# Kernel optimization log

Measured on AMD Instinct MI355X. Metric: run time of the kernel, lower is better.

The kernel has to match this reference:

```python
import jax, jax.numpy as jnp
import numpy as np
import math

D_MODEL = 1024
NUM_HEADS = 16
HEAD_DIM = D_MODEL // NUM_HEADS
N = 16384


def setup_inputs() -> dict:
    key = jax.random.key(0)
    ks = jax.random.split(key, 11)
    s = 1.0 / math.sqrt(D_MODEL)
    return {
        "q": jax.random.normal(ks[0], (N, D_MODEL), jnp.float32),
        "k": jax.random.normal(ks[1], (N, D_MODEL), jnp.float32),
        "v": jax.random.normal(ks[2], (N, D_MODEL), jnp.float32),
        "Wq": jax.random.normal(ks[3], (D_MODEL, D_MODEL), jnp.float32) * s,
        "bq": jnp.zeros((D_MODEL,), jnp.float32),
        "Wk": jax.random.normal(ks[4], (D_MODEL, D_MODEL), jnp.float32) * s,
        "bk": jnp.zeros((D_MODEL,), jnp.float32),
        "Wv": jax.random.normal(ks[5], (D_MODEL, D_MODEL), jnp.float32) * s,
        "bv": jnp.zeros((D_MODEL,), jnp.float32),
        "Wo": jax.random.normal(ks[6], (D_MODEL, D_MODEL), jnp.float32) * s,
        "bo": jnp.zeros((D_MODEL,), jnp.float32),
    }


def reference(q, k, v, Wq, bq, Wk, bk, Wv, bv, Wo, bo):
    scale = math.sqrt(HEAD_DIM)
    # Linear projections (torch Linear: x @ W.T + b), then view [N, H, Dh]
    qh = (q @ Wq.T + bq).reshape(-1, NUM_HEADS, HEAD_DIM)
    kh = (k @ Wk.T + bk).reshape(-1, NUM_HEADS, HEAD_DIM)
    vh = (v @ Wv.T + bv).reshape(-1, NUM_HEADS, HEAD_DIM)
    # NOTE: faithful to source — attention is over the HEADS axis per token:
    # scores [N, H, H]
    scores = jnp.einsum("nhd,ngd->nhg", qh, kh) / scale
    attn = jax.nn.softmax(scores, axis=-1)
    out = jnp.einsum("nhg,ngd->nhd", attn, vh).reshape(-1, D_MODEL)
    return out @ Wo.T + bo
```

## Files before the change

kernel.cpp:

```cpp
#include <hip/hip_runtime.h>

#define NTOK 16384
#define DM 1024
#define BM 128
#define BN 128
#define BK 64

typedef _Float16 h16;
typedef __attribute__((ext_vector_type(8))) _Float16 half8;
typedef __attribute__((ext_vector_type(4))) _Float16 half4;
typedef __attribute__((ext_vector_type(4))) float floatx4;

__device__ __forceinline__ unsigned lds_off(unsigned r, unsigned c) {
  return r * 128u + ((((c >> 3) ^ r) & 7u) << 4) + (c & 7u) * 2u;
}

__device__ __forceinline__ uint2 f4h4(float4 f) {
  unsigned short a = __builtin_bit_cast(unsigned short, (h16)f.x);
  unsigned short b = __builtin_bit_cast(unsigned short, (h16)f.y);
  unsigned short c = __builtin_bit_cast(unsigned short, (h16)f.z);
  unsigned short d = __builtin_bit_cast(unsigned short, (h16)f.w);
  uint2 r;
  r.x = (unsigned)a | ((unsigned)b << 16);
  r.y = (unsigned)c | ((unsigned)d << 16);
  return r;
}

template <bool AHALF, bool OHALF>
__global__ __launch_bounds__(256, 4) void gemm_h(const void* __restrict__ Aptr,
                                                 const float* __restrict__ W,
                                                 const float* __restrict__ bias,
                                                 void* __restrict__ Cptr) {
  __shared__ __align__(16) char smem[32768];
  char* Ap = smem;
  char* Bp = smem + 16384;

  const int tid = threadIdx.x;

  const int bid = (int)(blockIdx.x + gridDim.x * blockIdx.y);
  const int xcd = bid & 7, ch = bid >> 3;
  const int m0 = (xcd * 16 + (ch >> 3)) * BM;
  const int n0 = (ch & 7) * BN;

  const int lane = tid & 63;
  const int wave = tid >> 6;
  const int wm = (wave >> 1) * 64;
  const int wn = (wave & 1) * 64;
  const int fr = lane & 15;
  const int fq = lane >> 4;

  floatx4 acc[4][4] = {};

  const int rb = tid >> 4, c4 = tid & 15;
  const int rA = tid >> 3, c8 = tid & 7;

  const float* wg = W + (long)(n0 + rb) * DM + c4 * 4;
  const float* agf = AHALF ? nullptr : (const float*)Aptr + (long)(m0 + rb) * DM + c4 * 4;
  const h16* agh = AHALF ? (const h16*)Aptr + (long)(m0 + rA) * DM + c8 * 8 : nullptr;

  for (int kt = 0; kt < DM; kt += BK) {
    if constexpr (AHALF) {
#pragma unroll
      for (int i = 0; i < 4; ++i) {
        uint4 u = *(const uint4*)(agh + (long)i * 32 * DM + kt);
        *(uint4*)(Ap + lds_off(rA + i * 32, c8 * 8)) = u;
      }
    } else {
#pragma unroll
      for (int i = 0; i < 8; ++i) {
        float4 fa = *(const float4*)(agf + (long)i * 16 * DM + kt);
        *(uint2*)(Ap + lds_off(rb + i * 16, c4 * 4)) = f4h4(fa);
      }
    }
#pragma unroll
    for (int i = 0; i < 8; ++i) {
      float4 fb = *(const float4*)(wg + (long)i * 16 * DM + kt);
      *(uint2*)(Bp + lds_off(rb + i * 16, c4 * 4)) = f4h4(fb);
    }
    __syncthreads();

#pragma unroll
    for (int ks = 0; ks < 2; ++ks) {
      half8 af[4], bf[4];
#pragma unroll
      for (int i = 0; i < 4; ++i) {
        af[i] = *(half8*)(Ap + lds_off(wm + i * 16 + fr, ks * 32 + fq * 8));
        bf[i] = *(half8*)(Bp + lds_off(wn + i * 16 + fr, ks * 32 + fq * 8));
      }
#pragma unroll
      for (int mi = 0; mi < 4; ++mi)
#pragma unroll
        for (int ni = 0; ni < 4; ++ni)
          acc[mi][ni] = __builtin_amdgcn_mfma_f32_16x16x32_f16(af[mi], bf[ni], acc[mi][ni], 0, 0, 0);
    }
    __syncthreads();
  }

#pragma unroll
  for (int ni = 0; ni < 4; ++ni) {
    const int col = n0 + wn + ni * 16 + fr;
    const float bv = bias[col];
#pragma unroll
    for (int mi = 0; mi < 4; ++mi) {
      const int row0 = m0 + wm + mi * 16 + fq * 4;
#pragma unroll
      for (int j = 0; j < 4; ++j) {
        const float val = acc[mi][ni][j] + bv;
        if constexpr (OHALF)
          ((h16*)Cptr)[(long)(row0 + j) * DM + col] = (h16)val;
        else
          ((float*)Cptr)[(long)(row0 + j) * DM + col] = val;
      }
    }
  }
}

__global__ __launch_bounds__(256) void attn_heads_h(h16* __restrict__ Q,
                                                    const h16* __restrict__ K,
                                                    const h16* __restrict__ V) {
  __shared__ float qs[16][68];
  __shared__ float ks[16][68];
  __shared__ float vs[16][68];
  __shared__ float pw[16][17];
  const int t = blockIdx.x;
  const int tid = threadIdx.x;
  const long base = (long)t * DM + tid * 4;
  const int h = tid >> 4;
  const int d0 = (tid & 15) * 4;

  {
    half4 fq = *(const half4*)(Q + base);
    half4 fk = *(const half4*)(K + base);
    half4 fv = *(const half4*)(V + base);
    *(float4*)&qs[h][d0] = make_float4((float)fq[0], (float)fq[1], (float)fq[2], (float)fq[3]);
    *(float4*)&ks[h][d0] = make_float4((float)fk[0], (float)fk[1], (float)fk[2], (float)fk[3]);
    *(float4*)&vs[h][d0] = make_float4((float)fv[0], (float)fv[1], (float)fv[2], (float)fv[3]);
  }
  __syncthreads();

  const int g = tid & 15;
  float s = 0.f;
#pragma unroll
  for (int d = 0; d < 64; ++d) s += qs[h][d] * ks[g][d];
  s *= 0.125f;

  float mx = s;
#pragma unroll
  for (int off = 8; off > 0; off >>= 1) mx = fmaxf(mx, __shfl_xor(mx, off, 16));
  float e = __expf(s - mx);
  float den = e;
#pragma unroll
  for (int off = 8; off > 0; off >>= 1) den += __shfl_xor(den, off, 16);
  pw[h][g] = e / den;
  __syncthreads();

  float4 o = make_float4(0.f, 0.f, 0.f, 0.f);
#pragma unroll
  for (int g2 = 0; g2 < 16; ++g2) {
    const float p = pw[h][g2];
    o.x += p * vs[g2][d0 + 0];
    o.y += p * vs[g2][d0 + 1];
    o.z += p * vs[g2][d0 + 2];
    o.w += p * vs[g2][d0 + 3];
  }
  half4 oh;
  oh[0] = (h16)o.x; oh[1] = (h16)o.y; oh[2] = (h16)o.z; oh[3] = (h16)o.w;
  *(half4*)(Q + base) = oh;
}

extern "C" void kernel_launch(void* const* d_in, const int* in_sizes, int n_in,
                              void* d_out, int out_size, void* d_ws, size_t ws_size,
                              hipStream_t stream) {
  const float* q  = (const float*)d_in[0];
  const float* k  = (const float*)d_in[1];
  const float* v  = (const float*)d_in[2];
  const float* Wq = (const float*)d_in[3];
  const float* bq = (const float*)d_in[4];
  const float* Wk = (const float*)d_in[5];
  const float* bk = (const float*)d_in[6];
  const float* Wv = (const float*)d_in[7];
  const float* bv = (const float*)d_in[8];
  const float* Wo = (const float*)d_in[9];
  const float* bo = (const float*)d_in[10];

  h16* Qp = (h16*)d_ws;
  h16* Kp = Qp + (size_t)NTOK * DM;
  h16* Vp = Kp + (size_t)NTOK * DM;

  dim3 ggrid(DM / BN, NTOK / BM);
  dim3 gblk(256);

  gemm_h<false, true><<<ggrid, gblk, 0, stream>>>(q, Wq, bq, Qp);
  gemm_h<false, true><<<ggrid, gblk, 0, stream>>>(k, Wk, bk, Kp);
  gemm_h<false, true><<<ggrid, gblk, 0, stream>>>(v, Wv, bv, Vp);
  attn_heads_h<<<dim3(NTOK), gblk, 0, stream>>>(Qp, Kp, Vp);
  gemm_h<true, false><<<ggrid, gblk, 0, stream>>>(Qp, Wo, bo, (float*)d_out);
}
```

Baseline: 526.4 us.

## Pre-convert inputs and weights to fp16, load GEMM tiles via direct global-to-LDS

Adds separate conversion kernels that cast q/k/v and all four weight matrices to fp16 up front. The GEMM is rewritten to take fp16 operands only and to fill LDS with global_load_lds 16-byte direct copies using an XOR-swizzled lane mapping, instead of register-staged float loads converted in-loop. This is meant to cut per-tile conversion work and VGPR staging inside the GEMM, and to halve the bytes each GEMM reads. The cost is an extra full read/write pass over the activations and more workspace, with projection outputs reusing the converted input buffers.

```diff
diff --git a/kernel.cpp b/kernel.cpp
--- a/kernel.cpp
+++ b/kernel.cpp
@@ -15,22 +15,16 @@
   return r * 128u + ((((c >> 3) ^ r) & 7u) << 4) + (c & 7u) * 2u;
 }
 
-__device__ __forceinline__ uint2 f4h4(float4 f) {
-  unsigned short a = __builtin_bit_cast(unsigned short, (h16)f.x);
-  unsigned short b = __builtin_bit_cast(unsigned short, (h16)f.y);
-  unsigned short c = __builtin_bit_cast(unsigned short, (h16)f.z);
-  unsigned short d = __builtin_bit_cast(unsigned short, (h16)f.w);
-  uint2 r;
-  r.x = (unsigned)a | ((unsigned)b << 16);
-  r.y = (unsigned)c | ((unsigned)d << 16);
-  return r;
-}
-
-template <bool AHALF, bool OHALF>
-__global__ __launch_bounds__(256, 4) void gemm_h(const void* __restrict__ Aptr,
-                                                 const float* __restrict__ W,
-                                                 const float* __restrict__ bias,
-                                                 void* __restrict__ Cptr) {
+__device__ __forceinline__ void gload16(const h16* g, char* l) {
+  __builtin_amdgcn_global_load_lds((const __attribute__((address_space(1))) unsigned*)g,
+                                   (__attribute__((address_space(3))) unsigned*)l, 16, 0, 0);
+}
+
+template <bool OHALF>
+__global__ __launch_bounds__(256, 4) void gemm_hh(const h16* __restrict__ A,
+                                                  const h16* __restrict__ W,
+                                                  const float* __restrict__ bias,
+                                                  void* __restrict__ Cptr) {
   __shared__ __align__(16) char smem[32768];
   char* Ap = smem;
   char* Bp = smem + 16384;
@@ -51,31 +45,18 @@
 
   floatx4 acc[4][4] = {};
 
-  const int rb = tid >> 4, c4 = tid & 15;
-  const int rA = tid >> 3, c8 = tid & 7;
-
-  const float* wg = W + (long)(n0 + rb) * DM + c4 * 4;
-  const float* agf = AHALF ? nullptr : (const float*)Aptr + (long)(m0 + rb) * DM + c4 * 4;
-  const h16* agh = AHALF ? (const h16*)Aptr + (long)(m0 + rA) * DM + c8 * 8 : nullptr;
+  const int lr = lane >> 3;
+  const int lc = (lane & 7) ^ lr;
+  const h16* ag = A + (long)(m0 + wave * 32 + lr) * DM + lc * 8;
+  const h16* wg = W + (long)(n0 + wave * 32 + lr) * DM + lc * 8;
+  char* const alds = Ap + wave * 4096;
+  char* const blds = Bp + wave * 4096;
 
   for (int kt = 0; kt < DM; kt += BK) {
-    if constexpr (AHALF) {
-#pragma unroll
-      for (int i = 0; i < 4; ++i) {
-        uint4 u = *(const uint4*)(agh + (long)i * 32 * DM + kt);
-        *(uint4*)(Ap + lds_off(rA + i * 32, c8 * 8)) = u;
-      }
-    } else {
-#pragma unroll
-      for (int i = 0; i < 8; ++i) {
-        float4 fa = *(const float4*)(agf + (long)i * 16 * DM + kt);
-        *(uint2*)(Ap + lds_off(rb + i * 16, c4 * 4)) = f4h4(fa);
-      }
-    }
-#pragma unroll
-    for (int i = 0; i < 8; ++i) {
-      float4 fb = *(const float4*)(wg + (long)i * 16 * DM + kt);
-      *(uint2*)(Bp + lds_off(rb + i * 16, c4 * 4)) = f4h4(fb);
+#pragma unroll
+    for (int i = 0; i < 4; ++i) {
+      gload16(ag + (long)(i * 8) * DM + kt, alds + i * 1024);
+      gload16(wg + (long)(i * 8) * DM + kt, blds + i * 1024);
     }
     __syncthreads();
 
@@ -113,6 +94,35 @@
       }
     }
   }
+}
+
+__global__ __launch_bounds__(256) void cvt3(const float* __restrict__ a, const float* __restrict__ b,
+                                            const float* __restrict__ c, h16* __restrict__ oa,
+                                            h16* __restrict__ ob, h16* __restrict__ oc) {
+  const long i = ((long)blockIdx.x * 256 + threadIdx.x) * 8;
+  const float* s = blockIdx.y == 0 ? a : blockIdx.y == 1 ? b : c;
+  h16* d = blockIdx.y == 0 ? oa : blockIdx.y == 1 ? ob : oc;
+  float4 f0 = *(const float4*)(s + i);
+  float4 f1 = *(const float4*)(s + i + 4);
+  half8 h;
+  h[0] = (h16)f0.x; h[1] = (h16)f0.y; h[2] = (h16)f0.z; h[3] = (h16)f0.w;
+  h[4] = (h16)f1.x; h[5] = (h16)f1.y; h[6] = (h16)f1.z; h[7] = (h16)f1.w;
+  *(half8*)(d + i) = h;
+}
+
+__global__ __launch_bounds__(256) void cvtW(const float* __restrict__ a, const float* __restrict__ b,
+                                            const float* __restrict__ c, const float* __restrict__ e,
+                                            h16* __restrict__ oa, h16* __restrict__ ob,
+                                            h16* __restrict__ oc, h16* __restrict__ oe) {
+  const long i = ((long)blockIdx.x * 256 + threadIdx.x) * 8;
+  const float* s = blockIdx.y == 0 ? a : blockIdx.y == 1 ? b : blockIdx.y == 2 ? c : e;
+  h16* d = blockIdx.y == 0 ? oa : blockIdx.y == 1 ? ob : blockIdx.y == 2 ? oc : oe;
+  float4 f0 = *(const float4*)(s + i);
+  float4 f1 = *(const float4*)(s + i + 4);
+  half8 h;
+  h[0] = (h16)f0.x; h[1] = (h16)f0.y; h[2] = (h16)f0.z; h[3] = (h16)f0.w;
+  h[4] = (h16)f1.x; h[5] = (h16)f1.y; h[6] = (h16)f1.z; h[7] = (h16)f1.w;
+  *(half8*)(d + i) = h;
 }
 
 __global__ __launch_bounds__(256) void attn_heads_h(h16* __restrict__ Q,
@@ -183,16 +193,28 @@
   const float* Wo = (const float*)d_in[9];
   const float* bo = (const float*)d_in[10];
 
-  h16* Qp = (h16*)d_ws;
-  h16* Kp = Qp + (size_t)NTOK * DM;
-  h16* Vp = Kp + (size_t)NTOK * DM;
+  const size_t NE = (size_t)NTOK * DM;
+  const size_t WE = (size_t)DM * DM;
+  h16* qh  = (h16*)d_ws;
+  h16* kh  = qh + NE;
+  h16* vh  = kh + NE;
+  h16* Wqh = vh + NE;
+  h16* Wkh = Wqh + WE;
+  h16* Wvh = Wkh + WE;
+  h16* Woh = Wvh + WE;
+  h16* Qp  = Woh + WE;
+  h16* Kp  = qh;
+  h16* Vp  = kh;
 
   dim3 ggrid(DM / BN, NTOK / BM);
   dim3 gblk(256);
 
-  gemm_h<false, true><<<ggrid, gblk, 0, stream>>>(q, Wq, bq, Qp);
-  gemm_h<false, true><<<ggrid, gblk, 0, stream>>>(k, Wk, bk, Kp);
-  gemm_h<false, true><<<ggrid, gblk, 0, stream>>>(v, Wv, bv, Vp);
+  cvt3<<<dim3(NE / (256 * 8), 3), gblk, 0, stream>>>(q, k, v, qh, kh, vh);
+  cvtW<<<dim3(WE / (256 * 8), 4), gblk, 0, stream>>>(Wq, Wk, Wv, Wo, Wqh, Wkh, Wvh, Woh);
+
+  gemm_hh<true><<<ggrid, gblk, 0, stream>>>(qh, Wqh, bq, Qp);
+  gemm_hh<true><<<ggrid, gblk, 0, stream>>>(kh, Wkh, bk, Kp);
+  gemm_hh<true><<<ggrid, gblk, 0, stream>>>(vh, Wvh, bv, Vp);
   attn_heads_h<<<dim3(NTOK), gblk, 0, stream>>>(Qp, Kp, Vp);
-  gemm_h<true, false><<<ggrid, gblk, 0, stream>>>(Qp, Wo, bo, (float*)d_out);
-}
+  gemm_hh<false><<<ggrid, gblk, 0, stream>>>(Qp, Woh, bo, (float*)d_out);
+}
```

Result: faster. 448.7 us (-14.8%).

## Double-buffer GEMM tiles with direct global-to-LDS loads and pre-converted fp16 weights

Applied to the files above, without the earlier changes.

Adds a separate kernel that converts the four weight matrices to fp16 once per call. The GEMM then loads B tiles, and A tiles in the fp16 case, straight into LDS with global_load_lds, using an XOR-swizzled lane mapping. LDS is double-buffered (64KB) so the next tile's loads overlap the current tile's MFMAs, and one of the two barriers per iteration is dropped. In exchange, occupancy is lowered to 2 blocks per CU, and there is an extra launch plus extra workspace for the fp16 weights.

```diff
diff --git a/kernel.cpp b/kernel.cpp
--- a/kernel.cpp
+++ b/kernel.cpp
@@ -26,14 +26,35 @@
   return r;
 }
 
+__device__ __forceinline__ void gload16(const h16* g, char* l) {
+  __builtin_amdgcn_global_load_lds((const __attribute__((address_space(1))) unsigned*)g,
+                                   (__attribute__((address_space(3))) unsigned*)l, 16, 0, 0);
+}
+
+__device__ __forceinline__ void mfma_tile(const char* Ap, const char* Bp, int wm, int wn,
+                                          int fr, int fq, floatx4 (&acc)[4][4]) {
+#pragma unroll
+  for (int ks = 0; ks < 2; ++ks) {
+    half8 af[4], bf[4];
+#pragma unroll
+    for (int i = 0; i < 4; ++i) {
+      af[i] = *(const half8*)(Ap + lds_off(wm + i * 16 + fr, ks * 32 + fq * 8));
+      bf[i] = *(const half8*)(Bp + lds_off(wn + i * 16 + fr, ks * 32 + fq * 8));
+    }
+#pragma unroll
+    for (int mi = 0; mi < 4; ++mi)
+#pragma unroll
+      for (int ni = 0; ni < 4; ++ni)
+        acc[mi][ni] = __builtin_amdgcn_mfma_f32_16x16x32_f16(af[mi], bf[ni], acc[mi][ni], 0, 0, 0);
+  }
+}
+
 template <bool AHALF, bool OHALF>
-__global__ __launch_bounds__(256, 4) void gemm_h(const void* __restrict__ Aptr,
-                                                 const float* __restrict__ W,
+__global__ __launch_bounds__(256, 2) void gemm_p(const void* __restrict__ Aptr,
+                                                 const h16* __restrict__ W,
                                                  const float* __restrict__ bias,
                                                  void* __restrict__ Cptr) {
-  __shared__ __align__(16) char smem[32768];
-  char* Ap = smem;
-  char* Bp = smem + 16384;
+  __shared__ __align__(16) char smem[65536];
 
   const int tid = threadIdx.x;
 
@@ -51,50 +72,60 @@
 
   floatx4 acc[4][4] = {};
 
+  const int lr = lane >> 3;
+  const int lc = (lane & 7) ^ lr;
+  const h16* wg = W + (long)(n0 + wave * 32 + lr) * DM + lc * 8;
+  const h16* agh = AHALF ? (const h16*)Aptr + (long)(m0 + wave * 32 + lr) * DM + lc * 8 : nullptr;
+
   const int rb = tid >> 4, c4 = tid & 15;
-  const int rA = tid >> 3, c8 = tid & 7;
-
-  const float* wg = W + (long)(n0 + rb) * DM + c4 * 4;
   const float* agf = AHALF ? nullptr : (const float*)Aptr + (long)(m0 + rb) * DM + c4 * 4;
-  const h16* agh = AHALF ? (const h16*)Aptr + (long)(m0 + rA) * DM + c8 * 8 : nullptr;
-
-  for (int kt = 0; kt < DM; kt += BK) {
+  float4 areg[8];
+
+  auto issueB = [&](int kt, int buf) {
+    char* bl = smem + 16384 + buf * 32768 + wave * 4096;
+#pragma unroll
+    for (int i = 0; i < 4; ++i) gload16(wg + (long)(i * 8) * DM + kt, bl + i * 1024);
+  };
+  auto issueA_h = [&](int kt, int buf) {
+    char* al = smem + buf * 32768 + wave * 4096;
+#pragma unroll
+    for (int i = 0; i < 4; ++i) gload16(agh + (long)(i * 8) * DM + kt, al + i * 1024);
+  };
+  auto loadA_f = [&](int kt) {
+#pragma unroll
+    for (int i = 0; i < 8; ++i) areg[i] = *(const float4*)(agf + (long)(i * 16) * DM + kt);
+  };
+  auto writeA_f = [&](int buf) {
+    char* al = smem + buf * 32768;
+#pragma unroll
+    for (int i = 0; i < 8; ++i)
+      *(uint2*)(al + lds_off(rb + i * 16, c4 * 4)) = f4h4(areg[i]);
+  };
+
+  issueB(0, 0);
+  if constexpr (AHALF) {
+    issueA_h(0, 0);
+  } else {
+    loadA_f(0);
+    writeA_f(0);
+  }
+  __syncthreads();
+
+  int cur = 0;
+  for (int kt = BK; kt < DM; kt += BK) {
+    issueB(kt, cur ^ 1);
     if constexpr (AHALF) {
-#pragma unroll
-      for (int i = 0; i < 4; ++i) {
-        uint4 u = *(const uint4*)(agh + (long)i * 32 * DM + kt);
-        *(uint4*)(Ap + lds_off(rA + i * 32, c8 * 8)) = u;
-      }
+      issueA_h(kt, cur ^ 1);
+      mfma_tile(smem + cur * 32768, smem + 16384 + cur * 32768, wm, wn, fr, fq, acc);
     } else {
-#pragma unroll
-      for (int i = 0; i < 8; ++i) {
-        float4 fa = *(const float4*)(agf + (long)i * 16 * DM + kt);
-        *(uint2*)(Ap + lds_off(rb + i * 16, c4 * 4)) = f4h4(fa);
-      }
-    }
-#pragma unroll
-    for (int i = 0; i < 8; ++i) {
-      float4 fb = *(const float4*)(wg + (long)i * 16 * DM + kt);
-      *(uint2*)(Bp + lds_off(rb + i * 16, c4 * 4)) = f4h4(fb);
+      loadA_f(kt);
+      mfma_tile(smem + cur * 32768, smem + 16384 + cur * 32768, wm, wn, fr, fq, acc);
+      writeA_f(cur ^ 1);
     }
     __syncthreads();
-
-#pragma unroll
-    for (int ks = 0; ks < 2; ++ks) {
-      half8 af[4], bf[4];
-#pragma unroll
-      for (int i = 0; i < 4; ++i) {
-        af[i] = *(half8*)(Ap + lds_off(wm + i * 16 + fr, ks * 32 + fq * 8));
-        bf[i] = *(half8*)(Bp + lds_off(wn + i * 16 + fr, ks * 32 + fq * 8));
-      }
-#pragma unroll
-      for (int mi = 0; mi < 4; ++mi)
-#pragma unroll
-        for (int ni = 0; ni < 4; ++ni)
-          acc[mi][ni] = __builtin_amdgcn_mfma_f32_16x16x32_f16(af[mi], bf[ni], acc[mi][ni], 0, 0, 0);
-    }
-    __syncthreads();
-  }
+    cur ^= 1;
+  }
+  mfma_tile(smem + cur * 32768, smem + 16384 + cur * 32768, wm, wn, fr, fq, acc);
 
 #pragma unroll
   for (int ni = 0; ni < 4; ++ni) {
@@ -113,6 +144,21 @@
       }
     }
   }
+}
+
+__global__ __launch_bounds__(256) void cvtW(const float* __restrict__ a, const float* __restrict__ b,
+                                            const float* __restrict__ c, const float* __restrict__ e,
+                                            h16* __restrict__ oa, h16* __restrict__ ob,
+                                            h16* __restrict__ oc, h16* __restrict__ oe) {
+  const long i = ((long)blockIdx.x * 256 + threadIdx.x) * 8;
+  const float* s = blockIdx.y == 0 ? a : blockIdx.y == 1 ? b : blockIdx.y == 2 ? c : e;
+  h16* d = blockIdx.y == 0 ? oa : blockIdx.y == 1 ? ob : blockIdx.y == 2 ? oc : oe;
+  float4 f0 = *(const float4*)(s + i);
+  float4 f1 = *(const float4*)(s + i + 4);
+  half8 h;
+  h[0] = (h16)f0.x; h[1] = (h16)f0.y; h[2] = (h16)f0.z; h[3] = (h16)f0.w;
+  h[4] = (h16)f1.x; h[5] = (h16)f1.y; h[6] = (h16)f1.z; h[7] = (h16)f1.w;
+  *(half8*)(d + i) = h;
 }
 
 __global__ __launch_bounds__(256) void attn_heads_h(h16* __restrict__ Q,
@@ -183,16 +229,23 @@
   const float* Wo = (const float*)d_in[9];
   const float* bo = (const float*)d_in[10];
 
-  h16* Qp = (h16*)d_ws;
-  h16* Kp = Qp + (size_t)NTOK * DM;
-  h16* Vp = Kp + (size_t)NTOK * DM;
+  const size_t WE = (size_t)DM * DM;
+  h16* Wqh = (h16*)d_ws;
+  h16* Wkh = Wqh + WE;
+  h16* Wvh = Wkh + WE;
+  h16* Woh = Wvh + WE;
+  h16* Qp  = Woh + WE;
+  h16* Kp  = Qp + (size_t)NTOK * DM;
+  h16* Vp  = Kp + (size_t)NTOK * DM;
 
   dim3 ggrid(DM / BN, NTOK / BM);
   dim3 gblk(256);
 
-  gemm_h<false, true><<<ggrid, gblk, 0, stream>>>(q, Wq, bq, Qp);
-  gemm_h<false, true><<<ggrid, gblk, 0, stream>>>(k, Wk, bk, Kp);
-  gemm_h<false, true><<<ggrid, gblk, 0, stream>>>(v, Wv, bv, Vp);
+  cvtW<<<dim3(WE / (256 * 8), 4), gblk, 0, stream>>>(Wq, Wk, Wv, Wo, Wqh, Wkh, Wvh, Woh);
+
+  gemm_p<false, true><<<ggrid, gblk, 0, stream>>>(q, Wqh, bq, Qp);
+  gemm_p<false, true><<<ggrid, gblk, 0, stream>>>(k, Wkh, bk, Kp);
+  gemm_p<false, true><<<ggrid, gblk, 0, stream>>>(v, Wvh, bv, Vp);
   attn_heads_h<<<dim3(NTOK), gblk, 0, stream>>>(Qp, Kp, Vp);
-  gemm_h<true, false><<<ggrid, gblk, 0, stream>>>(Qp, Wo, bo, (float*)d_out);
-}
+  gemm_p<true, false><<<ggrid, gblk, 0, stream>>>(Qp, Woh, bo, (float*)d_out);
+}
```

Result: no change. 534.8 us (+1.6%).
